# Optimization experiments

Hardware: AMD Instinct MI355X
Metric: run time of the kernel (lower is better)

## Reference

```python
import jax, jax.numpy as jnp
import numpy as np

B, S, D = 2, 2048, 512
E, K = 8, 2
H = 4 * D  # expert_dim
EPS = 1e-10


def setup_inputs() -> dict:
    key = jax.random.key(0)
    ks = jax.random.split(key, 5)
    scale = 1.0 / np.sqrt(D)
    return {
        "x": jax.random.normal(ks[0], (B, S, D), dtype=jnp.float32),
        "w_router": jax.random.normal(ks[1], (D, E), dtype=jnp.float32) * scale,
        "w_gate": jax.random.normal(ks[2], (D, E * H), dtype=jnp.float32) * scale,
        "w_up": jax.random.normal(ks[3], (D, E * H), dtype=jnp.float32) * scale,
        "w_down": jax.random.normal(ks[4], (H, D), dtype=jnp.float32) * (1.0 / np.sqrt(H)),
    }


def reference(x, w_router, w_gate, w_up, w_down):
    b, s, d = x.shape
    n = b * s
    xf = x.reshape(n, d)

    # Router: softmax over experts, pick top-k, renormalize
    router_probs = jax.nn.softmax(xf @ w_router, axis=-1)          # [N, E]
    top_p, top_i = jax.lax.top_k(router_probs, K)                  # [N, K]
    top_p = top_p / (top_p.sum(axis=-1, keepdims=True) + EPS)

    # Dense all-expert gate/up projections (as in original module)
    gate = jax.nn.silu(xf @ w_gate).reshape(n, E, H)               # [N, E, H]
    up = (xf @ w_up).reshape(n, E, H)                              # [N, E, H]

    # Gather per-token top-k expert slices and combine
    sel_gate = jnp.take_along_axis(gate, top_i[:, :, None], axis=1)  # [N, K, H]
    sel_up = jnp.take_along_axis(up, top_i[:, :, None], axis=1)      # [N, K, H]
    combined = jnp.sum(top_p[:, :, None] * sel_gate * sel_up, axis=1)  # [N, H]

    out = (combined @ w_down).reshape(b, s, d)

    # Load-balancing aux loss
    expert_probs = router_probs.mean(axis=0)                       # [E]
    lb_loss = E * jnp.sum(expert_probs * jnp.log(expert_probs * E + EPS))
    return out, lb_loss
```

## Files before the change

### kernel.cpp

```cpp
#include <hip/hip_runtime.h>
#include <hip/hip_bf16.h>

#define N_TOK 4096
#define D_DIM 512
#define E_NUM 8
#define H_DIM 2048
#define RB_NUM 256
#define TP_NUM 8704

typedef __attribute__((ext_vector_type(8))) short short8;
typedef __attribute__((ext_vector_type(4))) float f32x4;

__device__ inline short f2bs(float f) {
  __hip_bfloat16 h = __float2bfloat16(f);
  return *reinterpret_cast<short*>(&h);
}

__device__ inline void llds16(const short* g, short* l) {
  __builtin_amdgcn_global_load_lds(
      (const __attribute__((address_space(1))) void*)g,
      (__attribute__((address_space(3))) void*)l, 16, 0, 0);
}

__global__ void __launch_bounds__(256) prep_router_kernel(
    const float* __restrict__ wg, const float* __restrict__ wu,
    const float* __restrict__ wd, const float* __restrict__ x,
    const float* __restrict__ wr, short* __restrict__ wgb,
    short* __restrict__ wub, short* __restrict__ wdb, short* __restrict__ xb,
    int* __restrict__ cnt_blk, int* __restrict__ tok_bkt,
    float* __restrict__ p_bkt, float* __restrict__ psum_blk) {
  int u = blockIdx.x;
  int tid = threadIdx.x;

  if (u >= RB_NUM) {
    __shared__ float tbuf[64][33];
    int v = u - RB_NUM;
    const float* in;
    short* op;
    int R, C, c0, r0;
    if (v < 8192) {
      in = (v < 4096) ? wg : wu;
      op = (v < 4096) ? wgb : wub;
      int w = v & 4095;
      R = D_DIM; C = E_NUM * H_DIM;
      c0 = (w & 511) * 32; r0 = (w >> 9) * 64;
    } else {
      in = wd; op = wdb;
      int w = v - 8192;
      R = H_DIM; C = D_DIM;
      c0 = (w & 15) * 32; r0 = (w >> 4) * 64;
    }
    int tx = tid & 31, ty = tid >> 5;
#pragma unroll
    for (int i = 0; i < 8; ++i)
      tbuf[ty + 8 * i][tx] = in[(size_t)(r0 + ty + 8 * i) * C + c0 + tx];
    __syncthreads();
#pragma unroll
    for (int i = 0; i < 4; ++i) {
      int cl = ty + 8 * i;
      unsigned lo = (unsigned short)f2bs(tbuf[2 * tx][cl]);
      unsigned hi = (unsigned short)f2bs(tbuf[2 * tx + 1][cl]);
      ((int*)op)[(((size_t)(c0 + cl) * R) + r0) / 2 + tx] = (int)(lo | (hi << 16));
    }
    return;
  }

  __shared__ float wr_t[E_NUM * D_DIM];
  __shared__ int h_cnt[E_NUM];
  __shared__ float psh[E_NUM];
  int rb = u;
  for (int i = tid; i < D_DIM * E_NUM; i += 256)
    wr_t[(i & 7) * D_DIM + (i >> 3)] = wr[i];
  if (tid < E_NUM) { h_cnt[tid] = 0; psh[tid] = 0.f; }
  __syncthreads();

  int r = tid >> 4, pp = tid & 15;
  int t = rb * 16 + r;
  const float* xr0 = x + (size_t)t * D_DIM;
  short* xw0 = xb + (size_t)t * D_DIM;
  float acc[8] = {0, 0, 0, 0, 0, 0, 0, 0};
#pragma unroll
  for (int j = 0; j < 8; ++j) {
    int d = j * 64 + pp * 4;
    float4 xv = *(const float4*)(xr0 + d);
    short4 o;
    o.x = f2bs(xv.x); o.y = f2bs(xv.y); o.z = f2bs(xv.z); o.w = f2bs(xv.w);
    *(short4*)(xw0 + d) = o;
#pragma unroll
    for (int e = 0; e < 8; ++e) {
      float4 w = *(const float4*)&wr_t[e * D_DIM + d];
      acc[e] += xv.x * w.x + xv.y * w.y + xv.z * w.z + xv.w * w.w;
    }
  }
#pragma unroll
  for (int e = 0; e < 8; ++e) {
    acc[e] += __shfl_xor(acc[e], 1);
    acc[e] += __shfl_xor(acc[e], 2);
    acc[e] += __shfl_xor(acc[e], 4);
    acc[e] += __shfl_xor(acc[e], 8);
  }

  if (pp == 0) {
    float m = acc[0];
#pragma unroll
    for (int e = 1; e < 8; ++e) m = fmaxf(m, acc[e]);
    float p[8], s = 0.f;
#pragma unroll
    for (int e = 0; e < 8; ++e) { p[e] = expf(acc[e] - m); s += p[e]; }
    float inv = 1.f / s;
#pragma unroll
    for (int e = 0; e < 8; ++e) {
      p[e] *= inv;
      atomicAdd(&psh[e], p[e]);
    }
    int i0 = 0;
#pragma unroll
    for (int e = 1; e < 8; ++e) if (p[e] > p[i0]) i0 = e;
    int i1 = (i0 == 0) ? 1 : 0;
#pragma unroll
    for (int e = 0; e < 8; ++e) if (e != i0 && p[e] > p[i1]) i1 = e;
    float ps = p[i0] + p[i1] + 1e-10f;
    float q0 = p[i0] / ps, q1 = p[i1] / ps;
    int l0 = atomicAdd(&h_cnt[i0], 1);
    int l1 = atomicAdd(&h_cnt[i1], 1);
    tok_bkt[i0 * (RB_NUM * 16) + rb * 16 + l0] = t * 2 + 0;
    p_bkt[i0 * (RB_NUM * 16) + rb * 16 + l0] = q0;
    tok_bkt[i1 * (RB_NUM * 16) + rb * 16 + l1] = t * 2 + 1;
    p_bkt[i1 * (RB_NUM * 16) + rb * 16 + l1] = q1;
  }
  __syncthreads();
  if (tid < E_NUM) {
    cnt_blk[rb * 8 + tid] = h_cnt[tid];
    psum_blk[rb * 8 + tid] = psh[tid];
  }
}

__global__ void __launch_bounds__(256, 2) moe_gateup_kernel(
    const short* __restrict__ xb, const short* __restrict__ wg,
    const short* __restrict__ wu, const int* __restrict__ cnt_blk,
    const int* __restrict__ tok_bkt, const float* __restrict__ p_bkt,
    const float* __restrict__ psum_blk, short* __restrict__ act,
    float* __restrict__ out_loss) {
  int e = blockIdx.z;
  int tid = threadIdx.x;

  if (e == 8) {
    if (blockIdx.x || blockIdx.y) return;
    __shared__ float sums[8];
    if (tid < 8) sums[tid] = 0.f;
    __syncthreads();
#pragma unroll
    for (int ee = 0; ee < 8; ++ee)
      atomicAdd(&sums[ee], psum_blk[tid * 8 + ee]);
    __syncthreads();
    if (tid == 0) {
      float lb = 0.f;
#pragma unroll
      for (int ee = 0; ee < 8; ++ee) {
        float pe = sums[ee] / (float)N_TOK;
        lb += pe * logf(pe * 8.f + 1e-10f);
      }
      out_loss[0] = 8.f * lb;
    }
    return;
  }

  __shared__ __align__(16) short As[256 * 64];
  __shared__ __align__(16) short Bgs[64 * 64];
  __shared__ __align__(16) short Bus[64 * 64];
  __shared__ int scan[256];
  __shared__ int wsum[4];
  __shared__ int s_row[256];
  __shared__ float s_pr[256];

  int lane = tid & 63, wid = tid >> 6;

  {
    int c = cnt_blk[tid * 8 + e];
#pragma unroll
    for (int ofs = 1; ofs < 64; ofs <<= 1) {
      int v = __shfl_up(c, ofs);
      if (lane >= ofs) c += v;
    }
    if (lane == 63) wsum[wid] = c;
    __syncthreads();
    int pre = 0;
#pragma unroll
    for (int w = 0; w < 4; ++w) pre += (w < wid) ? wsum[w] : 0;
    scan[tid] = c + pre;
    __syncthreads();
  }
  int n_e = scan[255];
  int rt = blockIdx.y;
  if (rt * 256 >= n_e) return;
  int h0 = blockIdx.x * 64;

  {
    int r = rt * 256 + tid;
    int srow = -1;
    float spr = 0.f;
    if (r < n_e) {
      int lo = 0, hi = 255;
      while (lo < hi) { int mid = (lo + hi) >> 1; if (scan[mid] > r) hi = mid; else lo = mid + 1; }
      int prev = lo ? scan[lo - 1] : 0;
      int idx = e * (RB_NUM * 16) + lo * 16 + (r - prev);
      srow = tok_bkt[idx];
      spr = p_bkt[idx];
    }
    s_row[tid] = srow;
    s_pr[tid] = spr;
  }
  __syncthreads();

  int cg = (lane & 7) ^ (lane >> 3);
  const short* baseA[8];
  const short* baseB[4];
  short* ldsA = As + (size_t)wid * 64 * 64;
  short* ldsB;
#pragma unroll
  for (int jj = 0; jj < 8; ++jj) {
    int r = wid * 64 + jj * 8 + (lane >> 3);
    int row = s_row[r];
    int t = (row < 0) ? 0 : (row >> 1);
    baseA[jj] = xb + (size_t)t * D_DIM + cg * 8;
  }
  {
    const short* wB = ((wid & 2) ? wu : wg) + (size_t)e * H_DIM * D_DIM;
    int rb = (wid & 1) * 32;
    ldsB = ((wid & 2) ? Bus : Bgs) + rb * 64;
#pragma unroll
    for (int jj = 0; jj < 4; ++jj) {
      int h = h0 + rb + jj * 8 + (lane >> 3);
      baseB[jj] = wB + (size_t)h * D_DIM + cg * 8;
    }
  }

  int ml = lane & 15, quad = lane >> 4;
  int m0w = wid * 64;
  f32x4 accG[4][4], accU[4][4];
#pragma unroll
  for (int mf = 0; mf < 4; ++mf)
#pragma unroll
    for (int nf = 0; nf < 4; ++nf) {
      accG[mf][nf] = (f32x4){0, 0, 0, 0};
      accU[mf][nf] = (f32x4){0, 0, 0, 0};
    }

  for (int kt = 0; kt < D_DIM / 64; ++kt) {
    int kb = kt * 64;
#pragma unroll
    for (int jj = 0; jj < 8; ++jj)
      llds16(baseA[jj] + kb, ldsA + jj * 8 * 64);
#pragma unroll
    for (int jj = 0; jj < 4; ++jj)
      llds16(baseB[jj] + kb, ldsB + jj * 8 * 64);
    __syncthreads();
#pragma unroll
    for (int ks = 0; ks < 2; ++ks) {
      int cs = ((quad + ks * 4) ^ (ml & 7)) * 8;
      short8 a[4], bg[4], bu[4];
#pragma unroll
      for (int mf = 0; mf < 4; ++mf)
        a[mf] = *(const short8*)&As[(m0w + mf * 16 + ml) * 64 + cs];
#pragma unroll
      for (int nf = 0; nf < 4; ++nf) {
        bg[nf] = *(const short8*)&Bgs[(nf * 16 + ml) * 64 + cs];
        bu[nf] = *(const short8*)&Bus[(nf * 16 + ml) * 64 + cs];
      }
#pragma unroll
      for (int mf = 0; mf < 4; ++mf)
#pragma unroll
        for (int nf = 0; nf < 4; ++nf) {
          accG[mf][nf] = __builtin_amdgcn_mfma_f32_16x16x32_bf16(a[mf], bg[nf], accG[mf][nf], 0, 0, 0);
          accU[mf][nf] = __builtin_amdgcn_mfma_f32_16x16x32_bf16(a[mf], bu[nf], accU[mf][nf], 0, 0, 0);
        }
    }
    __syncthreads();
  }

#pragma unroll
  for (int mf = 0; mf < 4; ++mf)
#pragma unroll
    for (int r = 0; r < 4; ++r) {
      int rl = m0w + mf * 16 + quad * 4 + r;
      int arow = s_row[rl];
      if (arow >= 0) {
        float pr = s_pr[rl];
#pragma unroll
        for (int nf = 0; nf < 4; ++nf) {
          float g = accG[mf][nf][r], u = accU[mf][nf][r];
          float val = pr * (g / (1.f + __expf(-g))) * u;
          act[(size_t)arow * H_DIM + h0 + nf * 16 + ml] = f2bs(val);
        }
      }
    }
}

__global__ void __launch_bounds__(256, 3) down_kernel(
    const short* __restrict__ act, const short* __restrict__ wd,
    float* __restrict__ partial) {
  __shared__ __align__(16) short As[128 * 64];
  __shared__ __align__(16) short Bs[128 * 64];
  int d0 = blockIdx.x * 128;
  int t0 = blockIdx.y * 128;
  int ksb = blockIdx.z;
  int tid = threadIdx.x, lane = tid & 63, wid = tid >> 6;
  int cg = (lane & 7) ^ (lane >> 3);

  const short* baseA[4];
  const short* baseB[4];
  short* ldsA = As + (size_t)wid * 32 * 64;
  short* ldsB = Bs + (size_t)wid * 32 * 64;
#pragma unroll
  for (int jj = 0; jj < 4; ++jj) {
    int r = wid * 32 + jj * 8 + (lane >> 3);
    baseA[jj] = act + (size_t)(2 * (t0 + r)) * H_DIM + cg * 8;
    int d = d0 + wid * 32 + jj * 8 + (lane >> 3);
    baseB[jj] = wd + (size_t)d * H_DIM + cg * 8;
  }

  int ml = lane & 15, quad = lane >> 4;
  int m0w = (wid & 1) * 64, n0w = (wid >> 1) * 64;
  f32x4 acc[4][4];
#pragma unroll
  for (int mf = 0; mf < 4; ++mf)
#pragma unroll
    for (int nf = 0; nf < 4; ++nf) acc[mf][nf] = (f32x4){0, 0, 0, 0};

  for (int kt = ksb * 16; kt < ksb * 16 + 16; ++kt) {
    size_t offA = (size_t)(kt & 1) * H_DIM + (kt >> 1) * 64;
    int offB = (kt >> 1) * 64;
#pragma unroll
    for (int jj = 0; jj < 4; ++jj) {
      llds16(baseA[jj] + offA, ldsA + jj * 8 * 64);
      llds16(baseB[jj] + offB, ldsB + jj * 8 * 64);
    }
    __syncthreads();
#pragma unroll
    for (int ks = 0; ks < 2; ++ks) {
      int cs = ((quad + ks * 4) ^ (ml & 7)) * 8;
      short8 a[4], b[4];
#pragma unroll
      for (int mf = 0; mf < 4; ++mf)
        a[mf] = *(const short8*)&As[(m0w + mf * 16 + ml) * 64 + cs];
#pragma unroll
      for (int nf = 0; nf < 4; ++nf)
        b[nf] = *(const short8*)&Bs[(n0w + nf * 16 + ml) * 64 + cs];
#pragma unroll
      for (int mf = 0; mf < 4; ++mf)
#pragma unroll
        for (int nf = 0; nf < 4; ++nf)
          acc[mf][nf] = __builtin_amdgcn_mfma_f32_16x16x32_bf16(a[mf], b[nf], acc[mf][nf], 0, 0, 0);
    }
    __syncthreads();
  }

  float* pout = partial + (size_t)ksb * N_TOK * D_DIM;
#pragma unroll
  for (int mf = 0; mf < 4; ++mf)
#pragma unroll
    for (int r = 0; r < 4; ++r) {
      int t = t0 + m0w + mf * 16 + quad * 4 + r;
#pragma unroll
      for (int nf = 0; nf < 4; ++nf)
        pout[(size_t)t * D_DIM + d0 + n0w + nf * 16 + ml] = acc[mf][nf][r];
    }
}

__global__ void __launch_bounds__(256) reduce_kernel(
    const float* __restrict__ partial, float* __restrict__ out) {
  int i = blockIdx.x * 256 + threadIdx.x;
  const int Q = N_TOK * D_DIM / 4;
  const float4* p = (const float4*)partial;
  float4 a = p[i], b = p[i + Q], c = p[i + 2 * Q], d = p[i + 3 * Q];
  float4 r = {a.x + b.x + c.x + d.x, a.y + b.y + c.y + d.y,
              a.z + b.z + c.z + d.z, a.w + b.w + c.w + d.w};
  ((float4*)out)[i] = r;
}

extern "C" void kernel_launch(void* const* d_in, const int* in_sizes, int n_in,
                              void* d_out, int out_size, void* d_ws, size_t ws_size,
                              hipStream_t stream) {
  const float* x = (const float*)d_in[0];
  const float* wr = (const float*)d_in[1];
  const float* wg = (const float*)d_in[2];
  const float* wu = (const float*)d_in[3];
  const float* wd = (const float*)d_in[4];
  float* out = (float*)d_out;

  char* ws = (char*)d_ws;
  size_t off = 0;
  auto alloc = [&](size_t bytes) {
    char* p = ws + off;
    off += (bytes + 255) & ~(size_t)255;
    return p;
  };
  short* xb = (short*)alloc((size_t)N_TOK * D_DIM * 2);
  short* wgb = (short*)alloc((size_t)E_NUM * H_DIM * D_DIM * 2);
  short* wub = (short*)alloc((size_t)E_NUM * H_DIM * D_DIM * 2);
  short* wdb = (short*)alloc((size_t)D_DIM * H_DIM * 2);
  short* act = (short*)alloc((size_t)N_TOK * 2 * H_DIM * 2);
  float* partial = (float*)alloc((size_t)4 * N_TOK * D_DIM * 4);
  int* cnt_blk = (int*)alloc((size_t)RB_NUM * E_NUM * 4);
  int* tok_bkt = (int*)alloc((size_t)E_NUM * RB_NUM * 16 * 4);
  float* p_bkt = (float*)alloc((size_t)E_NUM * RB_NUM * 16 * 4);
  float* psum_blk = (float*)alloc((size_t)RB_NUM * E_NUM * 4);

  prep_router_kernel<<<RB_NUM + TP_NUM, 256, 0, stream>>>(
      wg, wu, wd, x, wr, wgb, wub, wdb, xb, cnt_blk, tok_bkt, p_bkt, psum_blk);
  moe_gateup_kernel<<<dim3(H_DIM / 64, N_TOK / 256, E_NUM + 1), 256, 0, stream>>>(
      xb, wgb, wub, cnt_blk, tok_bkt, p_bkt, psum_blk, act,
      out + (size_t)N_TOK * D_DIM);
  down_kernel<<<dim3(D_DIM / 128, N_TOK / 128, 4), 256, 0, stream>>>(
      act, wdb, partial);
  reduce_kernel<<<N_TOK * D_DIM / 4 / 256, 256, 0, stream>>>(partial, out);
}
```

Baseline: 210.6 us.

## Double-buffer LDS in gate/up and down GEMMs, drop split-K reduce

```diff
diff --git a/kernel.cpp b/kernel.cpp
--- a/kernel.cpp
+++ b/kernel.cpp
@@ -20,6 +20,11 @@
   __builtin_amdgcn_global_load_lds(
       (const __attribute__((address_space(1))) void*)g,
       (__attribute__((address_space(3))) void*)l, 16, 0, 0);
+}
+
+__device__ inline void pipeb() {
+  asm volatile("s_waitcnt vmcnt(0)" ::: "memory");
+  __builtin_amdgcn_s_barrier();
 }
 
 __global__ void __launch_bounds__(256) prep_router_kernel(
@@ -135,7 +140,7 @@
   }
 }
 
-__global__ void __launch_bounds__(256, 2) moe_gateup_kernel(
+__global__ void __launch_bounds__(256, 1) moe_gateup_kernel(
     const short* __restrict__ xb, const short* __restrict__ wg,
     const short* __restrict__ wu, const int* __restrict__ cnt_blk,
     const int* __restrict__ tok_bkt, const float* __restrict__ p_bkt,
@@ -165,9 +170,9 @@
     return;
   }
 
-  __shared__ __align__(16) short As[256 * 64];
-  __shared__ __align__(16) short Bgs[64 * 64];
-  __shared__ __align__(16) short Bus[64 * 64];
+  __shared__ __align__(16) short As[2][256 * 64];
+  __shared__ __align__(16) short Bgs[2][64 * 64];
+  __shared__ __align__(16) short Bus[2][64 * 64];
   __shared__ int scan[256];
   __shared__ int wsum[4];
   __shared__ int s_row[256];
@@ -215,8 +220,6 @@
   int cg = (lane & 7) ^ (lane >> 3);
   const short* baseA[8];
   const short* baseB[4];
-  short* ldsA = As + (size_t)wid * 64 * 64;
-  short* ldsB;
 #pragma unroll
   for (int jj = 0; jj < 8; ++jj) {
     int r = wid * 64 + jj * 8 + (lane >> 3);
@@ -224,10 +227,11 @@
     int t = (row < 0) ? 0 : (row >> 1);
     baseA[jj] = xb + (size_t)t * D_DIM + cg * 8;
   }
+  int ldsB_off = (wid & 1) * 2048;
+  short* ldsBbase = (wid & 2) ? &Bus[0][0] : &Bgs[0][0];
   {
     const short* wB = ((wid & 2) ? wu : wg) + (size_t)e * H_DIM * D_DIM;
     int rb = (wid & 1) * 32;
-    ldsB = ((wid & 2) ? Bus : Bgs) + rb * 64;
 #pragma unroll
     for (int jj = 0; jj < 4; ++jj) {
       int h = h0 + rb + jj * 8 + (lane >> 3);
@@ -246,26 +250,28 @@
       accU[mf][nf] = (f32x4){0, 0, 0, 0};
     }
 
-  for (int kt = 0; kt < D_DIM / 64; ++kt) {
+  auto stage = [&](int bi, int kt) {
     int kb = kt * 64;
 #pragma unroll
     for (int jj = 0; jj < 8; ++jj)
-      llds16(baseA[jj] + kb, ldsA + jj * 8 * 64);
+      llds16(baseA[jj] + kb, &As[bi][wid * 4096 + jj * 512]);
 #pragma unroll
     for (int jj = 0; jj < 4; ++jj)
-      llds16(baseB[jj] + kb, ldsB + jj * 8 * 64);
-    __syncthreads();
+      llds16(baseB[jj] + kb, ldsBbase + bi * 4096 + ldsB_off + jj * 512);
+  };
+
+  auto compute = [&](int cur) {
 #pragma unroll
     for (int ks = 0; ks < 2; ++ks) {
       int cs = ((quad + ks * 4) ^ (ml & 7)) * 8;
       short8 a[4], bg[4], bu[4];
 #pragma unroll
       for (int mf = 0; mf < 4; ++mf)
-        a[mf] = *(const short8*)&As[(m0w + mf * 16 + ml) * 64 + cs];
+        a[mf] = *(const short8*)&As[cur][(m0w + mf * 16 + ml) * 64 + cs];
 #pragma unroll
       for (int nf = 0; nf < 4; ++nf) {
-        bg[nf] = *(const short8*)&Bgs[(nf * 16 + ml) * 64 + cs];
-        bu[nf] = *(const short8*)&Bus[(nf * 16 + ml) * 64 + cs];
+        bg[nf] = *(const short8*)&Bgs[cur][(nf * 16 + ml) * 64 + cs];
+        bu[nf] = *(const short8*)&Bus[cur][(nf * 16 + ml) * 64 + cs];
       }
 #pragma unroll
       for (int mf = 0; mf < 4; ++mf)
@@ -275,8 +281,17 @@
           accU[mf][nf] = __builtin_amdgcn_mfma_f32_16x16x32_bf16(a[mf], bu[nf], accU[mf][nf], 0, 0, 0);
         }
     }
-    __syncthreads();
-  }
+  };
+
+  stage(0, 0);
+  pipeb();
+#pragma unroll
+  for (int kt = 0; kt < 7; ++kt) {
+    stage((kt + 1) & 1, kt + 1);
+    compute(kt & 1);
+    pipeb();
+  }
+  compute(1);
 
 #pragma unroll
   for (int mf = 0; mf < 4; ++mf)
@@ -296,86 +311,90 @@
     }
 }
 
-__global__ void __launch_bounds__(256, 3) down_kernel(
+__global__ void __launch_bounds__(256, 2) down_kernel(
     const short* __restrict__ act, const short* __restrict__ wd,
-    float* __restrict__ partial) {
-  __shared__ __align__(16) short As[128 * 64];
-  __shared__ __align__(16) short Bs[128 * 64];
-  int d0 = blockIdx.x * 128;
+    float* __restrict__ out) {
+  __shared__ __align__(16) short As[2][2][128 * 64];
+  __shared__ __align__(16) short Bs[2][64 * 64];
+  int d0 = blockIdx.x * 64;
   int t0 = blockIdx.y * 128;
-  int ksb = blockIdx.z;
   int tid = threadIdx.x, lane = tid & 63, wid = tid >> 6;
   int cg = (lane & 7) ^ (lane >> 3);
 
   const short* baseA[4];
-  const short* baseB[4];
-  short* ldsA = As + (size_t)wid * 32 * 64;
-  short* ldsB = Bs + (size_t)wid * 32 * 64;
+  const short* baseB[2];
 #pragma unroll
   for (int jj = 0; jj < 4; ++jj) {
     int r = wid * 32 + jj * 8 + (lane >> 3);
     baseA[jj] = act + (size_t)(2 * (t0 + r)) * H_DIM + cg * 8;
-    int d = d0 + wid * 32 + jj * 8 + (lane >> 3);
+  }
+#pragma unroll
+  for (int jj = 0; jj < 2; ++jj) {
+    int d = d0 + wid * 16 + jj * 8 + (lane >> 3);
     baseB[jj] = wd + (size_t)d * H_DIM + cg * 8;
   }
 
   int ml = lane & 15, quad = lane >> 4;
-  int m0w = (wid & 1) * 64, n0w = (wid >> 1) * 64;
-  f32x4 acc[4][4];
-#pragma unroll
-  for (int mf = 0; mf < 4; ++mf)
+  f32x4 acc[2][4];
+#pragma unroll
+  for (int mf = 0; mf < 2; ++mf)
 #pragma unroll
     for (int nf = 0; nf < 4; ++nf) acc[mf][nf] = (f32x4){0, 0, 0, 0};
 
-  for (int kt = ksb * 16; kt < ksb * 16 + 16; ++kt) {
-    size_t offA = (size_t)(kt & 1) * H_DIM + (kt >> 1) * 64;
-    int offB = (kt >> 1) * 64;
-#pragma unroll
-    for (int jj = 0; jj < 4; ++jj) {
-      llds16(baseA[jj] + offA, ldsA + jj * 8 * 64);
-      llds16(baseB[jj] + offB, ldsB + jj * 8 * 64);
-    }
-    __syncthreads();
+  auto stage = [&](int bi, int j) {
+    int hb = j * 64;
+#pragma unroll
+    for (int s = 0; s < 2; ++s)
+#pragma unroll
+      for (int jj = 0; jj < 4; ++jj)
+        llds16(baseA[jj] + (size_t)s * H_DIM + hb, &As[bi][s][wid * 2048 + jj * 512]);
+#pragma unroll
+    for (int jj = 0; jj < 2; ++jj)
+      llds16(baseB[jj] + hb, &Bs[bi][(wid * 16 + jj * 8) * 64]);
+  };
+
+  auto compute = [&](int bi) {
 #pragma unroll
     for (int ks = 0; ks < 2; ++ks) {
       int cs = ((quad + ks * 4) ^ (ml & 7)) * 8;
-      short8 a[4], b[4];
-#pragma unroll
-      for (int mf = 0; mf < 4; ++mf)
-        a[mf] = *(const short8*)&As[(m0w + mf * 16 + ml) * 64 + cs];
+      short8 b[4];
 #pragma unroll
       for (int nf = 0; nf < 4; ++nf)
-        b[nf] = *(const short8*)&Bs[(n0w + nf * 16 + ml) * 64 + cs];
-#pragma unroll
-      for (int mf = 0; mf < 4; ++mf)
-#pragma unroll
-        for (int nf = 0; nf < 4; ++nf)
-          acc[mf][nf] = __builtin_amdgcn_mfma_f32_16x16x32_bf16(a[mf], b[nf], acc[mf][nf], 0, 0, 0);
-    }
-    __syncthreads();
-  }
-
-  float* pout = partial + (size_t)ksb * N_TOK * D_DIM;
-#pragma unroll
-  for (int mf = 0; mf < 4; ++mf)
+        b[nf] = *(const short8*)&Bs[bi][(nf * 16 + ml) * 64 + cs];
+#pragma unroll
+      for (int s = 0; s < 2; ++s) {
+        short8 a[2];
+#pragma unroll
+        for (int mf = 0; mf < 2; ++mf)
+          a[mf] = *(const short8*)&As[bi][s][(wid * 32 + mf * 16 + ml) * 64 + cs];
+#pragma unroll
+        for (int mf = 0; mf < 2; ++mf)
+#pragma unroll
+          for (int nf = 0; nf < 4; ++nf)
+            acc[mf][nf] = __builtin_amdgcn_mfma_f32_16x16x32_bf16(a[mf], b[nf], acc[mf][nf], 0, 0, 0);
+      }
+    }
+  };
+
+  stage(0, 0);
+  pipeb();
+#pragma unroll 2
+  for (int j = 0; j < 31; ++j) {
+    stage((j + 1) & 1, j + 1);
+    compute(j & 1);
+    pipeb();
+  }
+  compute(1);
+
+#pragma unroll
+  for (int mf = 0; mf < 2; ++mf)
 #pragma unroll
     for (int r = 0; r < 4; ++r) {
-      int t = t0 + m0w + mf * 16 + quad * 4 + r;
+      int t = t0 + wid * 32 + mf * 16 + quad * 4 + r;
 #pragma unroll
       for (int nf = 0; nf < 4; ++nf)
-        pout[(size_t)t * D_DIM + d0 + n0w + nf * 16 + ml] = acc[mf][nf][r];
-    }
-}
-
-__global__ void __launch_bounds__(256) reduce_kernel(
-    const float* __restrict__ partial, float* __restrict__ out) {
-  int i = blockIdx.x * 256 + threadIdx.x;
-  const int Q = N_TOK * D_DIM / 4;
-  const float4* p = (const float4*)partial;
-  float4 a = p[i], b = p[i + Q], c = p[i + 2 * Q], d = p[i + 3 * Q];
-  float4 r = {a.x + b.x + c.x + d.x, a.y + b.y + c.y + d.y,
-              a.z + b.z + c.z + d.z, a.w + b.w + c.w + d.w};
-  ((float4*)out)[i] = r;
+        out[(size_t)t * D_DIM + d0 + nf * 16 + ml] = acc[mf][nf][r];
+    }
 }
 
 extern "C" void kernel_launch(void* const* d_in, const int* in_sizes, int n_in,
@@ -400,7 +419,6 @@
   short* wub = (short*)alloc((size_t)E_NUM * H_DIM * D_DIM * 2);
   short* wdb = (short*)alloc((size_t)D_DIM * H_DIM * 2);
   short* act = (short*)alloc((size_t)N_TOK * 2 * H_DIM * 2);
-  float* partial = (float*)alloc((size_t)4 * N_TOK * D_DIM * 4);
   int* cnt_blk = (int*)alloc((size_t)RB_NUM * E_NUM * 4);
   int* tok_bkt = (int*)alloc((size_t)E_NUM * RB_NUM * 16 * 4);
   float* p_bkt = (float*)alloc((size_t)E_NUM * RB_NUM * 16 * 4);
@@ -411,7 +429,5 @@
   moe_gateup_kernel<<<dim3(H_DIM / 64, N_TOK / 256, E_NUM + 1), 256, 0, stream>>>(
       xb, wgb, wub, cnt_blk, tok_bkt, p_bkt, psum_blk, act,
       out + (size_t)N_TOK * D_DIM);
-  down_kernel<<<dim3(D_DIM / 128, N_TOK / 128, 4), 256, 0, stream>>>(
-      act, wdb, partial);
-  reduce_kernel<<<N_TOK * D_DIM / 4 / 256, 256, 0, stream>>>(partial, out);
-}
+  down_kernel<<<dim3(D_DIM / 64, N_TOK / 128), 256, 0, stream>>>(act, wdb, out);
+}
```

After: 247.4 us. 17.5% more time.

## Precompute dense per-expert token lists and reuse weight tiles in down GEMM

Applied to the files above, without the earlier changes.

```diff
diff --git a/kernel.cpp b/kernel.cpp
--- a/kernel.cpp
+++ b/kernel.cpp
@@ -135,10 +135,37 @@
   }
 }
 
+__global__ void __launch_bounds__(256) route_pack_kernel(
+    const int* __restrict__ cnt_blk, const int* __restrict__ tok_bkt,
+    const float* __restrict__ p_bkt, int* __restrict__ dense_tok,
+    float* __restrict__ dense_p, int* __restrict__ n_tot) {
+  int e = blockIdx.x;
+  int tid = threadIdx.x, lane = tid & 63, wid = tid >> 6;
+  __shared__ int wsum[4];
+  int c = cnt_blk[tid * 8 + e];
+  int inc = c;
+#pragma unroll
+  for (int ofs = 1; ofs < 64; ofs <<= 1) {
+    int v = __shfl_up(inc, ofs);
+    if (lane >= ofs) inc += v;
+  }
+  if (lane == 63) wsum[wid] = inc;
+  __syncthreads();
+  int pre = 0;
+#pragma unroll
+  for (int w = 0; w < 4; ++w) pre += (w < wid) ? wsum[w] : 0;
+  int excl = inc + pre - c;
+  for (int i = 0; i < c; ++i) {
+    dense_tok[e * N_TOK + excl + i] = tok_bkt[e * (RB_NUM * 16) + tid * 16 + i];
+    dense_p[e * N_TOK + excl + i] = p_bkt[e * (RB_NUM * 16) + tid * 16 + i];
+  }
+  if (tid == 255) n_tot[e] = inc + pre;
+}
+
 __global__ void __launch_bounds__(256, 2) moe_gateup_kernel(
     const short* __restrict__ xb, const short* __restrict__ wg,
-    const short* __restrict__ wu, const int* __restrict__ cnt_blk,
-    const int* __restrict__ tok_bkt, const float* __restrict__ p_bkt,
+    const short* __restrict__ wu, const int* __restrict__ dense_tok,
+    const float* __restrict__ dense_p, const int* __restrict__ n_tot,
     const float* __restrict__ psum_blk, short* __restrict__ act,
     float* __restrict__ out_loss) {
   int e = blockIdx.z;
@@ -165,47 +192,26 @@
     return;
   }
 
+  int n_e = n_tot[e];
+  int rt = blockIdx.y;
+  if (rt * 256 >= n_e) return;
+  int h0 = blockIdx.x * 64;
+
   __shared__ __align__(16) short As[256 * 64];
   __shared__ __align__(16) short Bgs[64 * 64];
   __shared__ __align__(16) short Bus[64 * 64];
-  __shared__ int scan[256];
-  __shared__ int wsum[4];
   __shared__ int s_row[256];
   __shared__ float s_pr[256];
 
   int lane = tid & 63, wid = tid >> 6;
-
-  {
-    int c = cnt_blk[tid * 8 + e];
-#pragma unroll
-    for (int ofs = 1; ofs < 64; ofs <<= 1) {
-      int v = __shfl_up(c, ofs);
-      if (lane >= ofs) c += v;
-    }
-    if (lane == 63) wsum[wid] = c;
-    __syncthreads();
-    int pre = 0;
-#pragma unroll
-    for (int w = 0; w < 4; ++w) pre += (w < wid) ? wsum[w] : 0;
-    scan[tid] = c + pre;
-    __syncthreads();
-  }
-  int n_e = scan[255];
-  int rt = blockIdx.y;
-  if (rt * 256 >= n_e) return;
-  int h0 = blockIdx.x * 64;
 
   {
     int r = rt * 256 + tid;
     int srow = -1;
     float spr = 0.f;
     if (r < n_e) {
-      int lo = 0, hi = 255;
-      while (lo < hi) { int mid = (lo + hi) >> 1; if (scan[mid] > r) hi = mid; else lo = mid + 1; }
-      int prev = lo ? scan[lo - 1] : 0;
-      int idx = e * (RB_NUM * 16) + lo * 16 + (r - prev);
-      srow = tok_bkt[idx];
-      spr = p_bkt[idx];
+      srow = dense_tok[e * N_TOK + r];
+      spr = dense_p[e * N_TOK + r];
     }
     s_row[tid] = srow;
     s_pr[tid] = spr;
@@ -215,8 +221,6 @@
   int cg = (lane & 7) ^ (lane >> 3);
   const short* baseA[8];
   const short* baseB[4];
-  short* ldsA = As + (size_t)wid * 64 * 64;
-  short* ldsB;
 #pragma unroll
   for (int jj = 0; jj < 8; ++jj) {
     int r = wid * 64 + jj * 8 + (lane >> 3);
@@ -224,6 +228,7 @@
     int t = (row < 0) ? 0 : (row >> 1);
     baseA[jj] = xb + (size_t)t * D_DIM + cg * 8;
   }
+  short* ldsB;
   {
     const short* wB = ((wid & 2) ? wu : wg) + (size_t)e * H_DIM * D_DIM;
     int rb = (wid & 1) * 32;
@@ -250,10 +255,10 @@
     int kb = kt * 64;
 #pragma unroll
     for (int jj = 0; jj < 8; ++jj)
-      llds16(baseA[jj] + kb, ldsA + jj * 8 * 64);
+      llds16(baseA[jj] + kb, As + wid * 4096 + jj * 512);
 #pragma unroll
     for (int jj = 0; jj < 4; ++jj)
-      llds16(baseB[jj] + kb, ldsB + jj * 8 * 64);
+      llds16(baseB[jj] + kb, ldsB + jj * 512);
     __syncthreads();
 #pragma unroll
     for (int ks = 0; ks < 2; ++ks) {
@@ -299,7 +304,8 @@
 __global__ void __launch_bounds__(256, 3) down_kernel(
     const short* __restrict__ act, const short* __restrict__ wd,
     float* __restrict__ partial) {
-  __shared__ __align__(16) short As[128 * 64];
+  __shared__ __align__(16) short As0[128 * 64];
+  __shared__ __align__(16) short As1[128 * 64];
   __shared__ __align__(16) short Bs[128 * 64];
   int d0 = blockIdx.x * 128;
   int t0 = blockIdx.y * 128;
@@ -309,8 +315,6 @@
 
   const short* baseA[4];
   const short* baseB[4];
-  short* ldsA = As + (size_t)wid * 32 * 64;
-  short* ldsB = Bs + (size_t)wid * 32 * 64;
 #pragma unroll
   for (int jj = 0; jj < 4; ++jj) {
     int r = wid * 32 + jj * 8 + (lane >> 3);
@@ -327,30 +331,34 @@
 #pragma unroll
     for (int nf = 0; nf < 4; ++nf) acc[mf][nf] = (f32x4){0, 0, 0, 0};
 
-  for (int kt = ksb * 16; kt < ksb * 16 + 16; ++kt) {
-    size_t offA = (size_t)(kt & 1) * H_DIM + (kt >> 1) * 64;
-    int offB = (kt >> 1) * 64;
+  for (int j = 0; j < 8; ++j) {
+    int hb = (ksb * 8 + j) * 64;
 #pragma unroll
     for (int jj = 0; jj < 4; ++jj) {
-      llds16(baseA[jj] + offA, ldsA + jj * 8 * 64);
-      llds16(baseB[jj] + offB, ldsB + jj * 8 * 64);
-    }
-    __syncthreads();
-#pragma unroll
-    for (int ks = 0; ks < 2; ++ks) {
-      int cs = ((quad + ks * 4) ^ (ml & 7)) * 8;
-      short8 a[4], b[4];
-#pragma unroll
-      for (int mf = 0; mf < 4; ++mf)
-        a[mf] = *(const short8*)&As[(m0w + mf * 16 + ml) * 64 + cs];
-#pragma unroll
-      for (int nf = 0; nf < 4; ++nf)
-        b[nf] = *(const short8*)&Bs[(n0w + nf * 16 + ml) * 64 + cs];
-#pragma unroll
-      for (int mf = 0; mf < 4; ++mf)
+      llds16(baseA[jj] + hb, As0 + wid * 2048 + jj * 512);
+      llds16(baseA[jj] + H_DIM + hb, As1 + wid * 2048 + jj * 512);
+      llds16(baseB[jj] + hb, Bs + wid * 2048 + jj * 512);
+    }
+    __syncthreads();
+#pragma unroll
+    for (int s = 0; s < 2; ++s) {
+      const short* Asl = s ? As1 : As0;
+#pragma unroll
+      for (int ks = 0; ks < 2; ++ks) {
+        int cs = ((quad + ks * 4) ^ (ml & 7)) * 8;
+        short8 a[4], b[4];
+#pragma unroll
+        for (int mf = 0; mf < 4; ++mf)
+          a[mf] = *(const short8*)&Asl[(m0w + mf * 16 + ml) * 64 + cs];
 #pragma unroll
         for (int nf = 0; nf < 4; ++nf)
-          acc[mf][nf] = __builtin_amdgcn_mfma_f32_16x16x32_bf16(a[mf], b[nf], acc[mf][nf], 0, 0, 0);
+          b[nf] = *(const short8*)&Bs[(n0w + nf * 16 + ml) * 64 + cs];
+#pragma unroll
+        for (int mf = 0; mf < 4; ++mf)
+#pragma unroll
+          for (int nf = 0; nf < 4; ++nf)
+            acc[mf][nf] = __builtin_amdgcn_mfma_f32_16x16x32_bf16(a[mf], b[nf], acc[mf][nf], 0, 0, 0);
+      }
     }
     __syncthreads();
   }
@@ -405,11 +413,16 @@
   int* tok_bkt = (int*)alloc((size_t)E_NUM * RB_NUM * 16 * 4);
   float* p_bkt = (float*)alloc((size_t)E_NUM * RB_NUM * 16 * 4);
   float* psum_blk = (float*)alloc((size_t)RB_NUM * E_NUM * 4);
+  int* dense_tok = (int*)alloc((size_t)E_NUM * N_TOK * 4);
+  float* dense_p = (float*)alloc((size_t)E_NUM * N_TOK * 4);
+  int* n_tot = (int*)alloc((size_t)E_NUM * 4);
 
   prep_router_kernel<<<RB_NUM + TP_NUM, 256, 0, stream>>>(
       wg, wu, wd, x, wr, wgb, wub, wdb, xb, cnt_blk, tok_bkt, p_bkt, psum_blk);
+  route_pack_kernel<<<E_NUM, 256, 0, stream>>>(
+      cnt_blk, tok_bkt, p_bkt, dense_tok, dense_p, n_tot);
   moe_gateup_kernel<<<dim3(H_DIM / 64, N_TOK / 256, E_NUM + 1), 256, 0, stream>>>(
-      xb, wgb, wub, cnt_blk, tok_bkt, p_bkt, psum_blk, act,
+      xb, wgb, wub, dense_tok, dense_p, n_tot, psum_blk, act,
       out + (size_t)N_TOK * D_DIM);
   down_kernel<<<dim3(D_DIM / 128, N_TOK / 128, 4), 256, 0, stream>>>(
       act, wdb, partial);
```

Measured after the change: 206.2 us. 2.1% less time.
